# Optimization experiments

Hardware: AMD Instinct MI355X
Metric: run time of the kernel (lower is better)

Reference implementation:

```python
import jax, jax.numpy as jnp
import numpy as np
import math

N = 4096
E = 512          # hidden_dim
H = 8            # num_heads
MAX_STEPS = 100
D_TIME = E // 2  # 256
D_STAT = E // 4  # 128


def _time_encoding():
    # sinusoidal table [MAX_STEPS, D_TIME], matching the torch buffer
    pos = jnp.arange(MAX_STEPS, dtype=jnp.float32)[:, None]
    div = jnp.exp(jnp.arange(0, D_TIME, 2, dtype=jnp.float32) * (-math.log(10000.0) / D_TIME))
    ang = pos * div  # [MAX_STEPS, D_TIME//2]
    return jnp.stack([jnp.sin(ang), jnp.cos(ang)], axis=-1).reshape(MAX_STEPS, D_TIME)


def setup_inputs() -> dict:
    key = jax.random.key(0)
    ks = jax.random.split(key, 12)
    w = 0.02
    return {
        "x": jax.random.normal(ks[0], (N, E), jnp.float32),
        "derived_mask": jax.random.randint(ks[1], (N,), 0, 2, jnp.int32),
        "step_numbers": jax.random.randint(ks[2], (N,), 0, MAX_STEPS, jnp.int32),
        "status_embed": jax.random.normal(ks[3], (2, D_STAT), jnp.float32),
        "in_proj_w": jax.random.normal(ks[4], (3 * E, E), jnp.float32) * w,
        "in_proj_b": jnp.zeros((3 * E,), jnp.float32),
        "out_proj_w": jax.random.normal(ks[5], (E, E), jnp.float32) * w,
        "out_proj_b": jnp.zeros((E,), jnp.float32),
        "mlp_w": jax.random.normal(ks[6], (E, E + D_STAT + D_TIME), jnp.float32) * w,
        "mlp_b": jnp.zeros((E,), jnp.float32),
        "ln_gamma": jnp.ones((E,), jnp.float32),
        "ln_beta": jnp.zeros((E,), jnp.float32),
    }


def reference(x, derived_mask, step_numbers, status_embed, in_proj_w, in_proj_b,
              out_proj_w, out_proj_b, mlp_w, mlp_b, ln_gamma, ln_beta):
    n = x.shape[0]
    hd = E // H

    # --- multihead self-attention with dynamic step-based mask ---
    qkv = x @ in_proj_w.T + in_proj_b                      # [N, 3E]
    q, k, v = jnp.split(qkv, 3, axis=-1)
    q = q.reshape(n, H, hd).transpose(1, 0, 2)             # [H, N, hd]
    k = k.reshape(n, H, hd).transpose(1, 0, 2)
    v = v.reshape(n, H, hd).transpose(1, 0, 2)

    scores = jnp.einsum('hnd,hmd->hnm', q, k) / math.sqrt(hd)   # [H, N, N]
    # mask[i, j] = True  <=>  step[j] - step[i] < 0 (blocked, -inf)
    blocked = (step_numbers[None, :] - step_numbers[:, None]) < 0
    scores = jnp.where(blocked[None, :, :], jnp.float32(-1e9), scores)
    attn = jax.nn.softmax(scores, axis=-1)
    ctx = jnp.einsum('hnm,hmd->hnd', attn, v)              # [H, N, hd]
    ctx = ctx.transpose(1, 0, 2).reshape(n, E)
    x_att = ctx @ out_proj_w.T + out_proj_b                # [N, E]

    # --- embeddings ---
    status = status_embed[derived_mask]                    # [N, E/4]
    step_c = jnp.clip(step_numbers, 0, MAX_STEPS - 1)
    time_emb = _time_encoding()[step_c]                    # [N, E/2]

    # --- fused output MLP: Linear -> LayerNorm -> ReLU ---
    combined = jnp.concatenate([x_att, status, time_emb], axis=-1)  # [N, 7E/4]
    h = combined @ mlp_w.T + mlp_b                         # [N, E]
    mu = jnp.mean(h, axis=-1, keepdims=True)
    var = jnp.mean((h - mu) ** 2, axis=-1, keepdims=True)
    h = (h - mu) / jnp.sqrt(var + 1e-5) * ln_gamma + ln_beta
    out = jnp.maximum(h, 0.0)
    return x + out
```

## Files before the change

### kernel.cpp

```cpp
#include <hip/hip_runtime.h>
#include <hip/hip_bf16.h>
#include <math.h>

typedef __bf16 bf16x8 __attribute__((ext_vector_type(8)));
typedef __bf16 bf16x4 __attribute__((ext_vector_type(4)));
typedef float f32x4 __attribute__((ext_vector_type(4)));

#define N_TOK 4096
#define EDIM 512
#define NHEAD 8
#define HD 64
#define LDCOMB 896
#define NBIN 100
#define SPLITK 8
#define BK 64
#define NQT 32

#define NU_CVT 3264
#define NU_TC 64
#define NU_ADD 128
#define NU_TMAT 128
#define NB_PREP (NU_CVT + NU_TC + NU_ADD + NU_TMAT + 1)

__device__ __forceinline__ unsigned int pk2(float a, float b) {
    union { __bf16 h[2]; unsigned int u; } x;
    x.h[0] = (__bf16)a; x.h[1] = (__bf16)b;
    return x.u;
}

__global__ __launch_bounds__(256) void prep_kernel(
    const float* __restrict__ x, const float* __restrict__ w_in,
    const float* __restrict__ w_mlp, const float* __restrict__ w_out,
    const float* __restrict__ status, const float* __restrict__ out_b,
    const float* __restrict__ mlp_b, const int* __restrict__ steps,
    __bf16* __restrict__ x_bf, __bf16* __restrict__ wqkv_bf,
    __bf16* __restrict__ wmlp_bf, __bf16* __restrict__ woutT_bf,
    float* __restrict__ add2, __bf16* __restrict__ tmat,
    int* __restrict__ perm, int* __restrict__ sstep,
    int* __restrict__ bs_row, int* __restrict__ qinfo) {
    __shared__ float T[64][65];
    __shared__ int hist[NBIN];
    __shared__ int offs[NBIN];
    const int bid = blockIdx.x;
    const int tid = threadIdx.x;
    const int wave = tid >> 6, lane = tid & 63;

    if (bid < NU_CVT) {
        int i = bid * 256 + tid;
        const int n0 = N_TOK * EDIM / 4;
        const int n1 = 3 * EDIM * EDIM / 4;
        const float* src; __bf16* dst;
        if (i < n0)           { src = x; dst = x_bf; }
        else if (i < n0 + n1) { i -= n0; src = w_in; dst = wqkv_bf; }
        else                  { i -= n0 + n1; src = w_mlp; dst = wmlp_bf; }
        const float4 v = ((const float4*)src)[i];
        bf16x4 o;
        o[0] = (__bf16)v.x; o[1] = (__bf16)v.y; o[2] = (__bf16)v.z; o[3] = (__bf16)v.w;
        ((bf16x4*)dst)[i] = o;
    } else if (bid < NU_CVT + NU_TC) {
        const int b2 = bid - NU_CVT;
        const int m0 = (b2 >> 3) * 64, k0 = (b2 & 7) * 64;
        const int row = tid >> 2, c4 = (tid & 3) * 16;
        #pragma unroll
        for (int i = 0; i < 4; i++) {
            const float4 v = *(const float4*)&w_out[(size_t)(m0 + row) * EDIM + k0 + c4 + i * 4];
            T[row][c4 + i * 4 + 0] = v.x;
            T[row][c4 + i * 4 + 1] = v.y;
            T[row][c4 + i * 4 + 2] = v.z;
            T[row][c4 + i * 4 + 3] = v.w;
        }
        __syncthreads();
        const int kr = tid >> 2, m16 = (tid & 3) * 16;
        bf16x8 o0, o1;
        #pragma unroll
        for (int i = 0; i < 8; i++) o0[i] = (__bf16)T[m16 + i][kr];
        #pragma unroll
        for (int i = 0; i < 8; i++) o1[i] = (__bf16)T[m16 + 8 + i][kr];
        *(bf16x8*)&woutT_bf[(size_t)(k0 + kr) * EDIM + m0 + m16] = o0;
        *(bf16x8*)&woutT_bf[(size_t)(k0 + kr) * EDIM + m0 + m16 + 8] = o1;
    } else if (bid < NU_CVT + NU_TC + NU_ADD) {
        const int j = (bid - NU_CVT - NU_TC) * 4 + wave;
        const float* wr = w_mlp + (size_t)j * LDCOMB;
        const int k8 = lane * 8;
        const float4 wa = *(const float4*)&wr[k8], wb = *(const float4*)&wr[k8 + 4];
        const float4 oa = *(const float4*)&out_b[k8], ob = *(const float4*)&out_b[k8 + 4];
        float b = wa.x * oa.x + wa.y * oa.y + wa.z * oa.z + wa.w * oa.w +
                  wb.x * ob.x + wb.y * ob.y + wb.z * ob.z + wb.w * ob.w;
        const int c2 = lane * 2;
        const float w0 = wr[EDIM + c2], w1 = wr[EDIM + c2 + 1];
        float s0 = status[c2] * w0 + status[c2 + 1] * w1;
        float s1 = status[128 + c2] * w0 + status[129 + c2] * w1;
        #pragma unroll
        for (int m = 1; m < 64; m <<= 1) {
            b += __shfl_xor(b, m);
            s0 += __shfl_xor(s0, m);
            s1 += __shfl_xor(s1, m);
        }
        if (lane == 0) {
            const float bb = b + mlp_b[j];
            add2[j] = s0 + bb;
            add2[EDIM + j] = s1 + bb;
        }
    } else if (bid < NU_CVT + NU_TC + NU_ADD + NU_TMAT) {
        const int st = bid - NU_CVT - NU_TC - NU_ADD;
        const int c = tid;
        const int pp = c >> 1;
        const float div = expf((float)(2 * pp) * (-9.210340371976184f / 256.0f));
        const float ang = (float)st * div;
        tmat[st * 256 + c] = (__bf16)((c & 1) ? cosf(ang) : sinf(ang));
    } else {
        if (tid < NBIN) hist[tid] = 0;
        __syncthreads();
        for (int i = tid; i < N_TOK; i += 256)
            atomicAdd(&hist[min(max(steps[i], 0), NBIN - 1)], 1);
        __syncthreads();
        if (tid == 0) {
            int acc = 0;
            for (int s = 0; s < NBIN; s++) { offs[s] = acc; acc += hist[s]; }
        }
        __syncthreads();
        if (tid < NBIN) hist[tid] = offs[tid];
        __syncthreads();
        for (int i = tid; i < N_TOK; i += 256) {
            const int s = min(max(steps[i], 0), NBIN - 1);
            const int pos = atomicAdd(&offs[s], 1);
            perm[pos] = i;
            sstep[pos] = s;
        }
        __syncthreads();
        for (int q = tid; q < N_TOK; q += 256)
            bs_row[q] = hist[sstep[q]];
        __syncthreads();
        for (int qt = tid; qt < NQT; qt += 256) {
            qinfo[qt * 2] = bs_row[qt * 128] & ~(BK - 1);
            qinfo[qt * 2 + 1] = bs_row[qt * 128 + 127];
        }
    }
}

__global__ __launch_bounds__(256) void gemm2_kernel(const __bf16* __restrict__ x_bf,
                                                    const __bf16* __restrict__ wqkv_bf,
                                                    const float* __restrict__ b_in,
                                                    const int* __restrict__ perm,
                                                    __bf16* __restrict__ qs,
                                                    __bf16* __restrict__ ks,
                                                    __bf16* __restrict__ vt,
                                                    const __bf16* __restrict__ wmlp_bf,
                                                    const __bf16* __restrict__ woutT_bf,
                                                    __bf16* __restrict__ weff_bf,
                                                    const __bf16* __restrict__ tmat,
                                                    float* __restrict__ tv) {
    __shared__ __attribute__((aligned(16))) union {
        struct { __bf16 As[128][40]; __bf16 Bs[128][40]; } g;
        __bf16 T[128][72];
    } sm;
    __shared__ int pr[128];
    const int bid = blockIdx.x;
    const int tid = threadIdx.x;
    const int wave = tid >> 6, lane = tid & 63;
    const int wm = (wave >> 1) * 64, wn = (wave & 1) * 64;
    const int lr = lane & 15, lq = lane >> 4;

    const __bf16 *A, *B;
    int lda, ldb, bm, bn, K, mode;
    if (bid < 384) {
        A = x_bf; lda = EDIM; B = wqkv_bf; ldb = EDIM; K = EDIM; mode = 0;
        bm = (bid & 31) * 128; bn = (bid >> 5) * 128;
        if (tid < 128) pr[tid] = perm[bm + tid];
    } else if (bid < 400) {
        const int b2 = bid - 384;
        A = wmlp_bf; lda = LDCOMB; B = woutT_bf; ldb = EDIM; K = EDIM; mode = 1;
        bm = (b2 & 3) * 128; bn = (b2 >> 2) * 128;
    } else {
        const int b3 = bid - 400;
        A = tmat; lda = 256; B = wmlp_bf + 640; ldb = LDCOMB; K = 256; mode = 2;
        bm = 0; bn = b3 * 128;
    }

    f32x4 acc[4][4] = {};
    for (int k0 = 0; k0 < K; k0 += 32) {
        __syncthreads();
        #pragma unroll
        for (int c = tid; c < 512; c += 256) {
            const int row = c >> 2, k8 = (c & 3) * 8;
            const int arow = (mode == 0) ? pr[row] : (bm + row);
            *(bf16x8*)&sm.g.As[row][k8] = *(const bf16x8*)&A[(size_t)arow * lda + k0 + k8];
            *(bf16x8*)&sm.g.Bs[row][k8] = *(const bf16x8*)&B[(size_t)(bn + row) * ldb + k0 + k8];
        }
        __syncthreads();
        bf16x8 af[4], bfr[4];
        #pragma unroll
        for (int i = 0; i < 4; i++) {
            af[i]  = *(const bf16x8*)&sm.g.As[wm + i * 16 + lr][lq * 8];
            bfr[i] = *(const bf16x8*)&sm.g.Bs[wn + i * 16 + lr][lq * 8];
        }
        #pragma unroll
        for (int i = 0; i < 4; i++)
            #pragma unroll
            for (int j = 0; j < 4; j++)
                acc[i][j] = __builtin_amdgcn_mfma_f32_16x16x32_bf16(af[i], bfr[j], acc[i][j], 0, 0, 0);
    }

    if (mode == 1) {
        #pragma unroll
        for (int i = 0; i < 4; i++)
            #pragma unroll
            for (int j = 0; j < 4; j++) {
                const int col = bn + wn + j * 16 + lr;
                #pragma unroll
                for (int r = 0; r < 4; r++)
                    weff_bf[(size_t)(bm + wm + i * 16 + lq * 4 + r) * EDIM + col] =
                        (__bf16)acc[i][j][r];
            }
    } else if (mode == 2) {
        #pragma unroll
        for (int i = 0; i < 4; i++)
            #pragma unroll
            for (int j = 0; j < 4; j++) {
                const int col = bn + wn + j * 16 + lr;
                #pragma unroll
                for (int r = 0; r < 4; r++) {
                    const int row = wm + i * 16 + lq * 4 + r;
                    if (row < NBIN) tv[(size_t)row * EDIM + col] = acc[i][j][r];
                }
            }
    } else if (bn < 512) {
        const float SC = 0.125f * 1.44269504f;
        #pragma unroll
        for (int i = 0; i < 4; i++)
            #pragma unroll
            for (int j = 0; j < 4; j++) {
                const int col = bn + wn + j * 16 + lr;
                const float bv = b_in[col];
                #pragma unroll
                for (int r = 0; r < 4; r++)
                    qs[(size_t)(bm + wm + i * 16 + lq * 4 + r) * EDIM + col] =
                        (__bf16)((acc[i][j][r] + bv) * SC);
            }
    } else if (bn < 1024) {
        #pragma unroll
        for (int i = 0; i < 4; i++)
            #pragma unroll
            for (int j = 0; j < 4; j++) {
                const int col = bn + wn + j * 16 + lr;
                const float bv = b_in[col];
                #pragma unroll
                for (int r = 0; r < 4; r++)
                    ks[(size_t)(bm + wm + i * 16 + lq * 4 + r) * EDIM + (col - 512)] =
                        (__bf16)(acc[i][j][r] + bv);
            }
    } else {
        #pragma unroll
        for (int half = 0; half < 2; half++) {
            __syncthreads();
            if ((wave & 1) == half) {
                #pragma unroll
                for (int i = 0; i < 4; i++)
                    #pragma unroll
                    for (int j = 0; j < 4; j++) {
                        const float bv = b_in[bn + wn + j * 16 + lr];
                        #pragma unroll
                        for (int r = 0; r < 4; r++)
                            sm.T[wm + i * 16 + lq * 4 + r][j * 16 + lr] =
                                (__bf16)(acc[i][j][r] + bv);
                    }
            }
            __syncthreads();
            for (int u = tid; u < 1024; u += 256) {
                const int d = u & 63, t8 = (u >> 6) * 8;
                bf16x8 v;
                #pragma unroll
                for (int j = 0; j < 8; j++) v[j] = sm.T[t8 + j][d];
                const int dim = (bn - 1024) + half * 64 + d;
                *(bf16x8*)&vt[(size_t)dim * N_TOK + bm + t8] = v;
            }
        }
    }
}

__global__ __launch_bounds__(256, 4) void attn_kernel(const __bf16* __restrict__ qs,
                                                      const __bf16* __restrict__ ks,
                                                      const __bf16* __restrict__ vt,
                                                      const int* __restrict__ bs_row,
                                                      const int* __restrict__ qinfo,
                                                      __bf16* __restrict__ po,
                                                      float* __restrict__ pl) {
    __shared__ __attribute__((aligned(16))) __bf16 KV[2][2][64 * 64];

    const int h = blockIdx.x & 7;
    const int qtile = blockIdx.x >> 3;
    const int ck = blockIdx.y;
    const int tid = threadIdx.x, wave = tid >> 6, lane = tid & 63;
    const int lr = lane & 15, lq = lane >> 4;
    const int wq0 = qtile * 128 + wave * 32;

    const int kt0 = qinfo[qtile * 2];
    const int bs_blockmax = qinfo[qtile * 2 + 1];
    const int nt = (N_TOK - kt0) / BK;
    const int kta = kt0 + ((nt * ck) / SPLITK) * BK;
    const int ktb = kt0 + ((nt * (ck + 1)) / SPLITK) * BK;

    bf16x8 aq[2][2];
    int bsg[2];
    #pragma unroll
    for (int g = 0; g < 2; g++) {
        const __bf16* qrow = qs + (size_t)(wq0 + g * 16 + lr) * EDIM + h * HD;
        aq[g][0] = *(const bf16x8*)&qrow[lq * 8];
        aq[g][1] = *(const bf16x8*)&qrow[32 + lq * 8];
        bsg[g] = bs_row[wq0 + g * 16 + lr];
    }

    bf16x8 ones;
    #pragma unroll
    for (int i = 0; i < 8; i++) ones[i] = (__bf16)1.0f;

    f32x4 lacc[2] = {};
    f32x4 o[2][4] = {};

    const int ro = lane >> 3;
    const int sc = (lane & 7) ^ ro;
    const int rbase = wave * 16;

    auto stage = [&](int buf, int kt_s) {
        #pragma unroll
        for (int i = 0; i < 2; i++) {
            const int rs = rbase + i * 8;
            const __bf16* gk = ks + (size_t)(kt_s + rs + ro) * EDIM + h * HD + sc * 8;
            __builtin_amdgcn_global_load_lds(
                (const __attribute__((address_space(1))) unsigned int*)gk,
                (__attribute__((address_space(3))) unsigned int*)&KV[buf][0][rs * 64],
                16, 0, 0);
            const __bf16* gv = vt + (size_t)(h * HD + rs + ro) * N_TOK + kt_s + sc * 8;
            __builtin_amdgcn_global_load_lds(
                (const __attribute__((address_space(1))) unsigned int*)gv,
                (__attribute__((address_space(3))) unsigned int*)&KV[buf][1][rs * 64],
                16, 0, 0);
        }
    };

    const int cswz = lr & 7;
    const int c0 = lq ^ cswz;

    if (kta < ktb) stage(0, kta);
    __syncthreads();

    int cur = 0;
    for (int kt = kta; kt < ktb; kt += BK) {
        if (kt + BK < ktb) stage(cur ^ 1, kt + BK);
        const __bf16* Kl = &KV[cur][0][0];
        const __bf16* Vl = &KV[cur][1][0];

        unsigned int pk[2][4][2];
        #pragma unroll
        for (int t = 0; t < 4; t++) {
            const bf16x8 kb0 = *(const bf16x8*)&Kl[t * 1024 + lr * 64 + c0 * 8];
            const bf16x8 kb1 = *(const bf16x8*)&Kl[t * 1024 + lr * 64 + (c0 ^ 4) * 8];
            #pragma unroll
            for (int g = 0; g < 2; g++) {
                f32x4 s = {};
                s = __builtin_amdgcn_mfma_f32_16x16x32_bf16(kb0, aq[g][0], s, 0, 0, 0);
                s = __builtin_amdgcn_mfma_f32_16x16x32_bf16(kb1, aq[g][1], s, 0, 0, 0);
                if (kt < bs_blockmax) {
                    const int tokb = kt + t * 16 + lq * 4;
                    #pragma unroll
                    for (int r = 0; r < 4; r++)
                        if (tokb + r < bsg[g]) s[r] = -1e9f;
                }
                pk[g][t][0] = pk2(exp2f(s[0]), exp2f(s[1]));
                pk[g][t][1] = pk2(exp2f(s[2]), exp2f(s[3]));
            }
        }
        #pragma unroll
        for (int k2 = 0; k2 < 2; k2++) {
            bf16x8 ptB[2];
            #pragma unroll
            for (int g = 0; g < 2; g++) {
                unsigned int a0 = pk[g][k2 * 2][0], a1 = pk[g][k2 * 2][1];
                unsigned int b0 = pk[g][k2 * 2 + 1][0], b1 = pk[g][k2 * 2 + 1][1];
                asm("v_permlane32_swap_b32 %0, %1" : "+v"(a0), "+v"(b0));
                asm("v_permlane32_swap_b32 %0, %1" : "+v"(a1), "+v"(b1));
                const unsigned int x0 = (unsigned int)__shfl_xor((int)a0, 16);
                const unsigned int x1 = (unsigned int)__shfl_xor((int)a1, 16);
                const unsigned int y0 = (unsigned int)__shfl_xor((int)b0, 16);
                const unsigned int y1 = (unsigned int)__shfl_xor((int)b1, 16);
                union { unsigned int u[4]; bf16x8 v; } fr;
                if (lq & 1) {
                    fr.u[0] = y0; fr.u[1] = y1; fr.u[2] = b0; fr.u[3] = b1;
                } else {
                    fr.u[0] = a0; fr.u[1] = a1; fr.u[2] = x0; fr.u[3] = x1;
                }
                ptB[g] = fr.v;
                lacc[g] = __builtin_amdgcn_mfma_f32_16x16x32_bf16(ones, ptB[g], lacc[g], 0, 0, 0);
            }
            #pragma unroll
            for (int dt = 0; dt < 4; dt++) {
                const bf16x8 bv = *(const bf16x8*)&Vl[dt * 1024 + lr * 64 + (c0 ^ (k2 * 4)) * 8];
                o[0][dt] = __builtin_amdgcn_mfma_f32_16x16x32_bf16(bv, ptB[0], o[0][dt], 0, 0, 0);
                o[1][dt] = __builtin_amdgcn_mfma_f32_16x16x32_bf16(bv, ptB[1], o[1][dt], 0, 0, 0);
            }
        }
        __syncthreads();
        cur ^= 1;
    }

    __bf16* pob = po + (((size_t)(ck * NHEAD + h) * N_TOK) + wq0) * HD;
    #pragma unroll
    for (int g = 0; g < 2; g++) {
        #pragma unroll
        for (int dt = 0; dt < 4; dt++) {
            bf16x4 ov;
            #pragma unroll
            for (int r = 0; r < 4; r++) ov[r] = (__bf16)o[g][dt][r];
            *(bf16x4*)&pob[(size_t)(g * 16 + lr) * HD + dt * 16 + lq * 4] = ov;
        }
        if (lq == 0)
            pl[(size_t)(ck * NHEAD + h) * N_TOK + wq0 + g * 16 + lr] = lacc[g][0];
    }
}

__global__ __launch_bounds__(256) void combine_kernel(const __bf16* __restrict__ po,
                                                      const float* __restrict__ pl,
                                                      const int* __restrict__ perm,
                                                      __bf16* __restrict__ ctx) {
    const int e = blockIdx.x * 256 + threadIdx.x;
    const int q = e >> 7;
    const int col = (e & 127) * 4;
    const int h = col >> 6, d = col & 63;
    float s0 = 0.f, s1 = 0.f, s2 = 0.f, s3 = 0.f, l = 0.f;
    #pragma unroll
    for (int c = 0; c < SPLITK; c++) {
        const bf16x4 v = *(const bf16x4*)&po[(((size_t)(c * NHEAD + h) * N_TOK) + q) * HD + d];
        s0 += (float)v[0]; s1 += (float)v[1]; s2 += (float)v[2]; s3 += (float)v[3];
        l += pl[(size_t)(c * NHEAD + h) * N_TOK + q];
    }
    const float rl = 1.0f / l;
    bf16x4 o;
    o[0] = (__bf16)(s0 * rl); o[1] = (__bf16)(s1 * rl);
    o[2] = (__bf16)(s2 * rl); o[3] = (__bf16)(s3 * rl);
    *(bf16x4*)&ctx[(size_t)perm[q] * EDIM + col] = o;
}

__global__ __launch_bounds__(256) void gemm_fused(const __bf16* __restrict__ A,
                                                  const __bf16* __restrict__ B,
                                                  const int* __restrict__ dmask,
                                                  const int* __restrict__ steps,
                                                  const float* __restrict__ add2,
                                                  const float* __restrict__ tv,
                                                  float* __restrict__ C) {
    __shared__ __attribute__((aligned(16))) __bf16 As[128][40];
    __shared__ __attribute__((aligned(16))) __bf16 Bs[128][40];
    const int tid = threadIdx.x;
    const int wave = tid >> 6, lane = tid & 63;
    const int wm = (wave >> 1) * 64, wn = (wave & 1) * 64;
    const int bm = blockIdx.x * 128, bn = blockIdx.y * 128;
    const int lr = lane & 15, lq = lane >> 4;

    f32x4 acc[4][4] = {};
    for (int k0 = 0; k0 < EDIM; k0 += 32) {
        __syncthreads();
        #pragma unroll
        for (int c = tid; c < 512; c += 256) {
            const int row = c >> 2, k8 = (c & 3) * 8;
            *(bf16x8*)&As[row][k8] = *(const bf16x8*)&A[(size_t)(bm + row) * EDIM + k0 + k8];
            *(bf16x8*)&Bs[row][k8] = *(const bf16x8*)&B[(size_t)(bn + row) * EDIM + k0 + k8];
        }
        __syncthreads();
        bf16x8 af[4], bfr[4];
        #pragma unroll
        for (int i = 0; i < 4; i++) {
            af[i]  = *(const bf16x8*)&As[wm + i * 16 + lr][lq * 8];
            bfr[i] = *(const bf16x8*)&Bs[wn + i * 16 + lr][lq * 8];
        }
        #pragma unroll
        for (int i = 0; i < 4; i++)
            #pragma unroll
            for (int j = 0; j < 4; j++)
                acc[i][j] = __builtin_amdgcn_mfma_f32_16x16x32_bf16(af[i], bfr[j], acc[i][j], 0, 0, 0);
    }

    int dmr[4][4], str[4][4];
    #pragma unroll
    for (int i = 0; i < 4; i++)
        #pragma unroll
        for (int r = 0; r < 4; r++) {
            const int row = bm + wm + i * 16 + lq * 4 + r;
            dmr[i][r] = dmask[row];
            str[i][r] = min(max(steps[row], 0), NBIN - 1);
        }
    #pragma unroll
    for (int i = 0; i < 4; i++)
        #pragma unroll
        for (int j = 0; j < 4; j++) {
            const int col = bn + wn + j * 16 + lr;
            #pragma unroll
            for (int r = 0; r < 4; r++) {
                const int row = bm + wm + i * 16 + lq * 4 + r;
                C[(size_t)row * EDIM + col] = acc[i][j][r]
                    + add2[dmr[i][r] * EDIM + col] + tv[str[i][r] * EDIM + col];
            }
        }
}

__global__ __launch_bounds__(256) void ln_kernel(const float* __restrict__ h,
                                                 const float* __restrict__ x,
                                                 const float* __restrict__ gamma,
                                                 const float* __restrict__ beta,
                                                 float* __restrict__ out) {
    const int row = blockIdx.x * 4 + (threadIdx.x >> 6);
    const int lane = threadIdx.x & 63;
    const float* hr = h + (size_t)row * EDIM;
    float4 v0 = ((const float4*)hr)[lane];
    float4 v1 = ((const float4*)hr)[64 + lane];
    float sum = v0.x + v0.y + v0.z + v0.w + v1.x + v1.y + v1.z + v1.w;
    float sq = v0.x * v0.x + v0.y * v0.y + v0.z * v0.z + v0.w * v0.w +
               v1.x * v1.x + v1.y * v1.y + v1.z * v1.z + v1.w * v1.w;
    #pragma unroll
    for (int m = 1; m < 64; m <<= 1) {
        sum += __shfl_xor(sum, m);
        sq  += __shfl_xor(sq, m);
    }
    const float mean = sum * (1.0f / EDIM);
    const float var = sq * (1.0f / EDIM) - mean * mean;
    const float rstd = rsqrtf(var + 1e-5f);
    const float* xr = x + (size_t)row * EDIM;
    float* orow = out + (size_t)row * EDIM;
    #pragma unroll
    for (int half = 0; half < 2; half++) {
        const float4 v = half ? v1 : v0;
        const int cb = half * 256 + lane * 4;
        const float* vp = (const float*)&v;
        float4 res;
        float tmp[4];
        #pragma unroll
        for (int i = 0; i < 4; i++) {
            const int c = cb + i;
            float t = (vp[i] - mean) * rstd * gamma[c] + beta[c];
            t = fmaxf(t, 0.f);
            tmp[i] = xr[c] + t;
        }
        res.x = tmp[0]; res.y = tmp[1]; res.z = tmp[2]; res.w = tmp[3];
        ((float4*)orow)[cb >> 2] = res;
    }
}

extern "C" void kernel_launch(void* const* d_in, const int* in_sizes, int n_in,
                              void* d_out, int out_size, void* d_ws, size_t ws_size,
                              hipStream_t stream) {
    const float* x      = (const float*)d_in[0];
    const int*   dmask  = (const int*)d_in[1];
    const int*   steps  = (const int*)d_in[2];
    const float* status = (const float*)d_in[3];
    const float* w_in   = (const float*)d_in[4];
    const float* b_in   = (const float*)d_in[5];
    const float* w_out  = (const float*)d_in[6];
    const float* b_out  = (const float*)d_in[7];
    const float* w_mlp  = (const float*)d_in[8];
    const float* b_mlp  = (const float*)d_in[9];
    const float* gamma  = (const float*)d_in[10];
    const float* beta   = (const float*)d_in[11];
    float* out = (float*)d_out;

    char* ws = (char*)d_ws;
    size_t off = 0;
    auto alloc = [&](size_t bytes) {
        void* ptr = ws + off;
        off = (off + bytes + 255) & ~(size_t)255;
        return ptr;
    };
    __bf16* x_bf    = (__bf16*)alloc((size_t)N_TOK * EDIM * 2);
    __bf16* wqkv_bf = (__bf16*)alloc((size_t)3 * EDIM * EDIM * 2);
    __bf16* wmlp_bf = (__bf16*)alloc((size_t)EDIM * LDCOMB * 2);
    __bf16* woutT_bf= (__bf16*)alloc((size_t)EDIM * EDIM * 2);
    __bf16* weff_bf = (__bf16*)alloc((size_t)EDIM * EDIM * 2);
    __bf16* qs_bf   = (__bf16*)alloc((size_t)N_TOK * EDIM * 2);
    __bf16* ks_bf   = (__bf16*)alloc((size_t)N_TOK * EDIM * 2);
    __bf16* vt_bf   = (__bf16*)alloc((size_t)EDIM * N_TOK * 2);
    __bf16* ctx_bf  = (__bf16*)alloc((size_t)N_TOK * EDIM * 2);
    float*  h_f32   = (float*)alloc((size_t)N_TOK * EDIM * 4);
    int*    perm    = (int*)alloc(N_TOK * 4);
    int*    sstep   = (int*)alloc(N_TOK * 4);
    int*    bs_row  = (int*)alloc(N_TOK * 4);
    int*    qinfo   = (int*)alloc(128 * 4);
    __bf16* po      = (__bf16*)alloc((size_t)SPLITK * NHEAD * N_TOK * HD * 2);
    float*  pl      = (float*)alloc((size_t)SPLITK * NHEAD * N_TOK * 4);
    float*  add2    = (float*)alloc(2 * EDIM * 4);
    float*  tv      = (float*)alloc((size_t)NBIN * EDIM * 4);
    __bf16* tmat    = (__bf16*)alloc(128 * 256 * 2);

    prep_kernel<<<NB_PREP, 256, 0, stream>>>(
        x, w_in, w_mlp, w_out, status, b_out, b_mlp, steps,
        x_bf, wqkv_bf, wmlp_bf, woutT_bf, add2, tmat, perm, sstep, bs_row, qinfo);
    gemm2_kernel<<<404, 256, 0, stream>>>(
        x_bf, wqkv_bf, b_in, perm, qs_bf, ks_bf, vt_bf,
        wmlp_bf, woutT_bf, weff_bf, tmat, tv);
    attn_kernel<<<dim3(NQT * NHEAD, SPLITK), 256, 0, stream>>>(
        qs_bf, ks_bf, vt_bf, bs_row, qinfo, po, pl);
    combine_kernel<<<(N_TOK * EDIM) / 1024, 256, 0, stream>>>(po, pl, perm, ctx_bf);
    gemm_fused<<<dim3(N_TOK / 128, EDIM / 128), 256, 0, stream>>>(
        ctx_bf, weff_bf, dmask, steps, add2, tv, h_f32);
    ln_kernel<<<N_TOK / 4, 256, 0, stream>>>(h_f32, x, gamma, beta, out);
}
```

Before: 195.3 us.

## Load K/V fragments directly from global memory, dropping LDS staging in attention

Removes the double-buffered LDS staging of K and V tiles and its per-iteration barrier. Each wave now loads its MFMA K and V fragments straight from global memory into registers. The four waves of a block each load the same K/V data, so the design relies on L2/L1 to absorb the redundant global traffic, and there is no longer any explicit prefetch overlap. The launch bound is lowered from 4 to 2 blocks per CU so the compiler can use more registers for the loaded fragments.

```diff
diff --git a/kernel.cpp b/kernel.cpp
--- a/kernel.cpp
+++ b/kernel.cpp
@@ -278,15 +278,13 @@
     }
 }
 
-__global__ __launch_bounds__(256, 4) void attn_kernel(const __bf16* __restrict__ qs,
+__global__ __launch_bounds__(256, 2) void attn_kernel(const __bf16* __restrict__ qs,
                                                       const __bf16* __restrict__ ks,
                                                       const __bf16* __restrict__ vt,
                                                       const int* __restrict__ bs_row,
                                                       const int* __restrict__ qinfo,
                                                       __bf16* __restrict__ po,
                                                       float* __restrict__ pl) {
-    __shared__ __attribute__((aligned(16))) __bf16 KV[2][2][64 * 64];
-
     const int h = blockIdx.x & 7;
     const int qtile = blockIdx.x >> 3;
     const int ck = blockIdx.y;
@@ -317,49 +315,33 @@
     f32x4 lacc[2] = {};
     f32x4 o[2][4] = {};
 
-    const int ro = lane >> 3;
-    const int sc = (lane & 7) ^ ro;
-    const int rbase = wave * 16;
-
-    auto stage = [&](int buf, int kt_s) {
-        #pragma unroll
-        for (int i = 0; i < 2; i++) {
-            const int rs = rbase + i * 8;
-            const __bf16* gk = ks + (size_t)(kt_s + rs + ro) * EDIM + h * HD + sc * 8;
-            __builtin_amdgcn_global_load_lds(
-                (const __attribute__((address_space(1))) unsigned int*)gk,
-                (__attribute__((address_space(3))) unsigned int*)&KV[buf][0][rs * 64],
-                16, 0, 0);
-            const __bf16* gv = vt + (size_t)(h * HD + rs + ro) * N_TOK + kt_s + sc * 8;
-            __builtin_amdgcn_global_load_lds(
-                (const __attribute__((address_space(1))) unsigned int*)gv,
-                (__attribute__((address_space(3))) unsigned int*)&KV[buf][1][rs * 64],
-                16, 0, 0);
-        }
-    };
-
-    const int cswz = lr & 7;
-    const int c0 = lq ^ cswz;
-
-    if (kta < ktb) stage(0, kta);
-    __syncthreads();
-
-    int cur = 0;
+    const __bf16* kb = ks + h * HD;
+    const __bf16* vb = vt + (size_t)h * HD * N_TOK;
+
     for (int kt = kta; kt < ktb; kt += BK) {
-        if (kt + BK < ktb) stage(cur ^ 1, kt + BK);
-        const __bf16* Kl = &KV[cur][0][0];
-        const __bf16* Vl = &KV[cur][1][0];
+        bf16x8 vf[4][2];
+        #pragma unroll
+        for (int dt = 0; dt < 4; dt++) {
+            const __bf16* vrow = vb + (size_t)(dt * 16 + lr) * N_TOK + kt;
+            vf[dt][0] = *(const bf16x8*)&vrow[lq * 8];
+            vf[dt][1] = *(const bf16x8*)&vrow[32 + lq * 8];
+        }
+        bf16x8 kf[4][2];
+        #pragma unroll
+        for (int t = 0; t < 4; t++) {
+            const __bf16* krow = kb + (size_t)(kt + t * 16 + lr) * EDIM;
+            kf[t][0] = *(const bf16x8*)&krow[lq * 8];
+            kf[t][1] = *(const bf16x8*)&krow[32 + lq * 8];
+        }
 
         unsigned int pk[2][4][2];
         #pragma unroll
         for (int t = 0; t < 4; t++) {
-            const bf16x8 kb0 = *(const bf16x8*)&Kl[t * 1024 + lr * 64 + c0 * 8];
-            const bf16x8 kb1 = *(const bf16x8*)&Kl[t * 1024 + lr * 64 + (c0 ^ 4) * 8];
             #pragma unroll
             for (int g = 0; g < 2; g++) {
                 f32x4 s = {};
-                s = __builtin_amdgcn_mfma_f32_16x16x32_bf16(kb0, aq[g][0], s, 0, 0, 0);
-                s = __builtin_amdgcn_mfma_f32_16x16x32_bf16(kb1, aq[g][1], s, 0, 0, 0);
+                s = __builtin_amdgcn_mfma_f32_16x16x32_bf16(kf[t][0], aq[g][0], s, 0, 0, 0);
+                s = __builtin_amdgcn_mfma_f32_16x16x32_bf16(kf[t][1], aq[g][1], s, 0, 0, 0);
                 if (kt < bs_blockmax) {
                     const int tokb = kt + t * 16 + lq * 4;
                     #pragma unroll
@@ -394,13 +376,10 @@
             }
             #pragma unroll
             for (int dt = 0; dt < 4; dt++) {
-                const bf16x8 bv = *(const bf16x8*)&Vl[dt * 1024 + lr * 64 + (c0 ^ (k2 * 4)) * 8];
-                o[0][dt] = __builtin_amdgcn_mfma_f32_16x16x32_bf16(bv, ptB[0], o[0][dt], 0, 0, 0);
-                o[1][dt] = __builtin_amdgcn_mfma_f32_16x16x32_bf16(bv, ptB[1], o[1][dt], 0, 0, 0);
-            }
-        }
-        __syncthreads();
-        cur ^= 1;
+                o[0][dt] = __builtin_amdgcn_mfma_f32_16x16x32_bf16(vf[dt][k2], ptB[0], o[0][dt], 0, 0, 0);
+                o[1][dt] = __builtin_amdgcn_mfma_f32_16x16x32_bf16(vf[dt][k2], ptB[1], o[1][dt], 0, 0, 0);
+            }
+        }
     }
 
     __bf16* pob = po + (((size_t)(ck * NHEAD + h) * N_TOK) + wq0) * HD;
```

Result: slower. 233.6 us (+19.6%).

## Switch attention to 32x32x16 MFMA tiles with padded LDS and halve split-K

Applied to the files above, without the earlier changes.

The attention inner loop moves from 16x16x32 to 32x32x16 bf16 MFMA instructions. Each wave now owns 32 query rows in a single fragment, which simplifies the P-fragment transpose to permlane32 swaps without xor shuffles. LDS rows are padded (520-element groups) to change the bank mapping, and s_setprio is raised around the MFMA section. SPLITK drops from 8 to 4, so each block does more sequential work and the combine step has fewer partials to read. The risks are fewer blocks in flight and higher register pressure from the f32x16 accumulators.

```diff
diff --git a/kernel.cpp b/kernel.cpp
--- a/kernel.cpp
+++ b/kernel.cpp
@@ -5,6 +5,7 @@
 typedef __bf16 bf16x8 __attribute__((ext_vector_type(8)));
 typedef __bf16 bf16x4 __attribute__((ext_vector_type(4)));
 typedef float f32x4 __attribute__((ext_vector_type(4)));
+typedef float f32x16 __attribute__((ext_vector_type(16)));
 
 #define N_TOK 4096
 #define EDIM 512
@@ -12,7 +13,7 @@
 #define HD 64
 #define LDCOMB 896
 #define NBIN 100
-#define SPLITK 8
+#define SPLITK 4
 #define BK 64
 #define NQT 32
 
@@ -285,13 +286,13 @@
                                                       const int* __restrict__ qinfo,
                                                       __bf16* __restrict__ po,
                                                       float* __restrict__ pl) {
-    __shared__ __attribute__((aligned(16))) __bf16 KV[2][2][64 * 64];
+    __shared__ __attribute__((aligned(16))) __bf16 KVs[2][2][4160];
 
     const int h = blockIdx.x & 7;
     const int qtile = blockIdx.x >> 3;
     const int ck = blockIdx.y;
     const int tid = threadIdx.x, wave = tid >> 6, lane = tid & 63;
-    const int lr = lane & 15, lq = lane >> 4;
+    const int l31 = lane & 31, hi = lane >> 5;
     const int wq0 = qtile * 128 + wave * 32;
 
     const int kt0 = qinfo[qtile * 2];
@@ -300,46 +301,42 @@
     const int kta = kt0 + ((nt * ck) / SPLITK) * BK;
     const int ktb = kt0 + ((nt * (ck + 1)) / SPLITK) * BK;
 
-    bf16x8 aq[2][2];
-    int bsg[2];
-    #pragma unroll
-    for (int g = 0; g < 2; g++) {
-        const __bf16* qrow = qs + (size_t)(wq0 + g * 16 + lr) * EDIM + h * HD;
-        aq[g][0] = *(const bf16x8*)&qrow[lq * 8];
-        aq[g][1] = *(const bf16x8*)&qrow[32 + lq * 8];
-        bsg[g] = bs_row[wq0 + g * 16 + lr];
-    }
+    bf16x8 aq[4];
+    {
+        const __bf16* qrow = qs + (size_t)(wq0 + l31) * EDIM + h * HD;
+        #pragma unroll
+        for (int m = 0; m < 4; m++) aq[m] = *(const bf16x8*)&qrow[m * 16 + hi * 8];
+    }
+    const int bsq = bs_row[wq0 + l31];
 
     bf16x8 ones;
     #pragma unroll
     for (int i = 0; i < 8; i++) ones[i] = (__bf16)1.0f;
 
-    f32x4 lacc[2] = {};
-    f32x4 o[2][4] = {};
+    f32x16 lacc = {};
+    f32x16 o0 = {}, o1 = {};
 
     const int ro = lane >> 3;
     const int sc = (lane & 7) ^ ro;
-    const int rbase = wave * 16;
 
     auto stage = [&](int buf, int kt_s) {
         #pragma unroll
         for (int i = 0; i < 2; i++) {
-            const int rs = rbase + i * 8;
-            const __bf16* gk = ks + (size_t)(kt_s + rs + ro) * EDIM + h * HD + sc * 8;
+            const int g = wave * 2 + i;
+            const __bf16* gk = ks + (size_t)(kt_s + g * 8 + ro) * EDIM + h * HD + sc * 8;
             __builtin_amdgcn_global_load_lds(
                 (const __attribute__((address_space(1))) unsigned int*)gk,
-                (__attribute__((address_space(3))) unsigned int*)&KV[buf][0][rs * 64],
+                (__attribute__((address_space(3))) unsigned int*)&KVs[buf][0][g * 520],
                 16, 0, 0);
-            const __bf16* gv = vt + (size_t)(h * HD + rs + ro) * N_TOK + kt_s + sc * 8;
+            const __bf16* gv = vt + (size_t)(h * HD + g * 8 + ro) * N_TOK + kt_s + sc * 8;
             __builtin_amdgcn_global_load_lds(
                 (const __attribute__((address_space(1))) unsigned int*)gv,
-                (__attribute__((address_space(3))) unsigned int*)&KV[buf][1][rs * 64],
+                (__attribute__((address_space(3))) unsigned int*)&KVs[buf][1][g * 520],
                 16, 0, 0);
         }
     };
 
-    const int cswz = lr & 7;
-    const int c0 = lq ^ cswz;
+    #define LDOFF(r, c) (((r) >> 3) * 520 + ((r) & 7) * 64 + ((((c) ^ ((r) & 7))) << 3))
 
     if (kta < ktb) stage(0, kta);
     __syncthreads();
@@ -347,75 +344,65 @@
     int cur = 0;
     for (int kt = kta; kt < ktb; kt += BK) {
         if (kt + BK < ktb) stage(cur ^ 1, kt + BK);
-        const __bf16* Kl = &KV[cur][0][0];
-        const __bf16* Vl = &KV[cur][1][0];
-
-        unsigned int pk[2][4][2];
-        #pragma unroll
-        for (int t = 0; t < 4; t++) {
-            const bf16x8 kb0 = *(const bf16x8*)&Kl[t * 1024 + lr * 64 + c0 * 8];
-            const bf16x8 kb1 = *(const bf16x8*)&Kl[t * 1024 + lr * 64 + (c0 ^ 4) * 8];
-            #pragma unroll
-            for (int g = 0; g < 2; g++) {
-                f32x4 s = {};
-                s = __builtin_amdgcn_mfma_f32_16x16x32_bf16(kb0, aq[g][0], s, 0, 0, 0);
-                s = __builtin_amdgcn_mfma_f32_16x16x32_bf16(kb1, aq[g][1], s, 0, 0, 0);
-                if (kt < bs_blockmax) {
-                    const int tokb = kt + t * 16 + lq * 4;
-                    #pragma unroll
-                    for (int r = 0; r < 4; r++)
-                        if (tokb + r < bsg[g]) s[r] = -1e9f;
+        const __bf16* Kl = &KVs[cur][0][0];
+        const __bf16* Vl = &KVs[cur][1][0];
+
+        __builtin_amdgcn_s_setprio(1);
+        #pragma unroll
+        for (int t = 0; t < 2; t++) {
+            f32x16 s = {};
+            #pragma unroll
+            for (int m = 0; m < 4; m++) {
+                const bf16x8 kb = *(const bf16x8*)&Kl[LDOFF(t * 32 + l31, 2 * m + hi)];
+                s = __builtin_amdgcn_mfma_f32_32x32x16_bf16(kb, aq[m], s, 0, 0, 0);
+            }
+            if (kt < bs_blockmax) {
+                const int tokb = kt + t * 32 + 4 * hi;
+                #pragma unroll
+                for (int r = 0; r < 16; r++) {
+                    const int tok = tokb + (r & 3) + 8 * (r >> 2);
+                    if (tok < bsq) s[r] = -1e9f;
                 }
-                pk[g][t][0] = pk2(exp2f(s[0]), exp2f(s[1]));
-                pk[g][t][1] = pk2(exp2f(s[2]), exp2f(s[3]));
-            }
-        }
-        #pragma unroll
-        for (int k2 = 0; k2 < 2; k2++) {
-            bf16x8 ptB[2];
-            #pragma unroll
-            for (int g = 0; g < 2; g++) {
-                unsigned int a0 = pk[g][k2 * 2][0], a1 = pk[g][k2 * 2][1];
-                unsigned int b0 = pk[g][k2 * 2 + 1][0], b1 = pk[g][k2 * 2 + 1][1];
-                asm("v_permlane32_swap_b32 %0, %1" : "+v"(a0), "+v"(b0));
-                asm("v_permlane32_swap_b32 %0, %1" : "+v"(a1), "+v"(b1));
-                const unsigned int x0 = (unsigned int)__shfl_xor((int)a0, 16);
-                const unsigned int x1 = (unsigned int)__shfl_xor((int)a1, 16);
-                const unsigned int y0 = (unsigned int)__shfl_xor((int)b0, 16);
-                const unsigned int y1 = (unsigned int)__shfl_xor((int)b1, 16);
-                union { unsigned int u[4]; bf16x8 v; } fr;
-                if (lq & 1) {
-                    fr.u[0] = y0; fr.u[1] = y1; fr.u[2] = b0; fr.u[3] = b1;
-                } else {
-                    fr.u[0] = a0; fr.u[1] = a1; fr.u[2] = x0; fr.u[3] = x1;
-                }
-                ptB[g] = fr.v;
-                lacc[g] = __builtin_amdgcn_mfma_f32_16x16x32_bf16(ones, ptB[g], lacc[g], 0, 0, 0);
-            }
-            #pragma unroll
-            for (int dt = 0; dt < 4; dt++) {
-                const bf16x8 bv = *(const bf16x8*)&Vl[dt * 1024 + lr * 64 + (c0 ^ (k2 * 4)) * 8];
-                o[0][dt] = __builtin_amdgcn_mfma_f32_16x16x32_bf16(bv, ptB[0], o[0][dt], 0, 0, 0);
-                o[1][dt] = __builtin_amdgcn_mfma_f32_16x16x32_bf16(bv, ptB[1], o[1][dt], 0, 0, 0);
-            }
-        }
+            }
+            unsigned int pk[8];
+            #pragma unroll
+            for (int m = 0; m < 8; m++)
+                pk[m] = pk2(exp2f(s[2 * m]), exp2f(s[2 * m + 1]));
+            asm("v_permlane32_swap_b32 %0, %1" : "+v"(pk[0]), "+v"(pk[2]));
+            asm("v_permlane32_swap_b32 %0, %1" : "+v"(pk[1]), "+v"(pk[3]));
+            asm("v_permlane32_swap_b32 %0, %1" : "+v"(pk[4]), "+v"(pk[6]));
+            asm("v_permlane32_swap_b32 %0, %1" : "+v"(pk[5]), "+v"(pk[7]));
+            union { unsigned int u[4]; bf16x8 v; } f0, f1;
+            f0.u[0] = pk[0]; f0.u[1] = pk[1]; f0.u[2] = pk[2]; f0.u[3] = pk[3];
+            f1.u[0] = pk[4]; f1.u[1] = pk[5]; f1.u[2] = pk[6]; f1.u[3] = pk[7];
+            lacc = __builtin_amdgcn_mfma_f32_32x32x16_bf16(ones, f0.v, lacc, 0, 0, 0);
+            lacc = __builtin_amdgcn_mfma_f32_32x32x16_bf16(ones, f1.v, lacc, 0, 0, 0);
+            #pragma unroll
+            for (int h2 = 0; h2 < 2; h2++) {
+                const bf16x8 va = *(const bf16x8*)&Vl[LDOFF(l31, 4 * t + 2 * h2 + hi)];
+                const bf16x8 vb = *(const bf16x8*)&Vl[LDOFF(32 + l31, 4 * t + 2 * h2 + hi)];
+                const bf16x8 pf = h2 ? f1.v : f0.v;
+                o0 = __builtin_amdgcn_mfma_f32_32x32x16_bf16(va, pf, o0, 0, 0, 0);
+                o1 = __builtin_amdgcn_mfma_f32_32x32x16_bf16(vb, pf, o1, 0, 0, 0);
+            }
+        }
+        __builtin_amdgcn_s_setprio(0);
         __syncthreads();
         cur ^= 1;
     }
-
-    __bf16* pob = po + (((size_t)(ck * NHEAD + h) * N_TOK) + wq0) * HD;
-    #pragma unroll
-    for (int g = 0; g < 2; g++) {
-        #pragma unroll
-        for (int dt = 0; dt < 4; dt++) {
-            bf16x4 ov;
-            #pragma unroll
-            for (int r = 0; r < 4; r++) ov[r] = (__bf16)o[g][dt][r];
-            *(bf16x4*)&pob[(size_t)(g * 16 + lr) * HD + dt * 16 + lq * 4] = ov;
-        }
-        if (lq == 0)
-            pl[(size_t)(ck * NHEAD + h) * N_TOK + wq0 + g * 16 + lr] = lacc[g][0];
-    }
+    #undef LDOFF
+
+    __bf16* pob = po + (((size_t)(ck * NHEAD + h) * N_TOK) + wq0 + l31) * HD;
+    #pragma unroll
+    for (int rg = 0; rg < 4; rg++) {
+        bf16x4 ova, ovb;
+        #pragma unroll
+        for (int r = 0; r < 4; r++) { ova[r] = (__bf16)o0[rg * 4 + r]; ovb[r] = (__bf16)o1[rg * 4 + r]; }
+        *(bf16x4*)&pob[rg * 8 + 4 * hi] = ova;
+        *(bf16x4*)&pob[32 + rg * 8 + 4 * hi] = ovb;
+    }
+    if (hi == 0)
+        pl[(size_t)(ck * NHEAD + h) * N_TOK + wq0 + l31] = lacc[0];
 }
 
 __global__ __launch_bounds__(256) void combine_kernel(const __bf16* __restrict__ po,
```

After: 198.9 us. Within noise of the previous version (+1.8%).
